# Performance work log

Measured on AMD Instinct MI355X. Metric: run time of the kernel, lower is better.

Reference implementation:

```python
import jax, jax.numpy as jnp
import numpy as np

WS = 8        # window_size
NH = 12       # num_heads


def setup_inputs() -> dict:
    key = jax.random.key(0)
    ks = jax.random.split(key, 9)
    B, C, H, W = 4, 384, 128, 128
    s = 1.0 / np.sqrt(C)
    x = jax.random.normal(ks[0], (B, C, H, W), dtype=jnp.float32)
    Wq = jax.random.normal(ks[1], (C, C), dtype=jnp.float32) * s
    bq = jax.random.normal(ks[2], (C,), dtype=jnp.float32) * 0.01
    Wk = jax.random.normal(ks[3], (C, C), dtype=jnp.float32) * s
    bk = jax.random.normal(ks[4], (C,), dtype=jnp.float32) * 0.01
    Wv = jax.random.normal(ks[5], (C, C), dtype=jnp.float32) * s
    bv = jax.random.normal(ks[6], (C,), dtype=jnp.float32) * 0.01
    Wp = jax.random.normal(ks[7], (C, C), dtype=jnp.float32) * s
    bp = jax.random.normal(ks[8], (C,), dtype=jnp.float32) * 0.01
    return {"x": x, "Wq": Wq, "bq": bq, "Wk": Wk, "bk": bk,
            "Wv": Wv, "bv": bv, "Wp": Wp, "bp": bp}


def reference(x, Wq, bq, Wk, bk, Wv, bv, Wp, bp):
    B, C, H, W = x.shape
    ws2 = WS * WS
    dk = C // NH
    scale = dk ** -0.5

    # window_partition: flat row-major reshape (same semantics as torch's
    # reshape on a contiguous [B,C,H,W] tensor), then permute+view.
    p = x.reshape(B, H // WS, WS, W // WS, WS, C)
    p = jnp.transpose(p, (0, 5, 1, 3, 2, 4))          # [B, C, H/ws, W/ws, ws, ws]
    p = p.reshape(B, C, -1, ws2)                       # [B, C, nW, ws*ws]

    def conv1x1(w, b):  # 1x1 Conv2d on [B,C,nW,ws2]
        return jnp.einsum('bcnw,oc->bonw', p, w) + b[None, :, None, None]

    def heads(t):  # permute(0,2,3,1).contiguous().reshape -> [B, NH, nW, ws2, dk]
        t = jnp.transpose(t, (0, 2, 3, 1))             # [B, nW, ws2, C]
        return t.reshape(B, NH, -1, ws2, dk)           # row-major reinterpretation

    q = heads(conv1x1(Wq, bq))
    k = heads(conv1x1(Wk, bk))
    v = heads(conv1x1(Wv, bv))

    scores = jnp.einsum('bhnqd,bhnkd->bhnqk', q, k) * scale
    attn = jax.nn.softmax(scores, axis=-1)
    o = jnp.einsum('bhnqk,bhnkd->bhnqd', attn, v)      # [B, NH, nW, ws2, dk]
    o = o.reshape(B, -1, ws2, C)                       # [B, nW, ws2, C]

    # window_unpartition
    u = o.reshape(B, -1, WS, WS, C)
    u = jnp.transpose(u, (0, 4, 1, 2, 3))              # [B, C, nW, ws, ws]
    u = u.reshape(B, C, H, W)

    y = jnp.einsum('bchw,oc->bohw', u, Wp) + bp[None, :, None, None]
    return y
```

## Files before the change

### kernel.cpp

```cpp
#include <hip/hip_runtime.h>
#include <hip/hip_bf16.h>
#include <stdint.h>


typedef __bf16 bf16_t;
typedef __bf16 bf16x8 __attribute__((ext_vector_type(8)));
typedef __bf16 bf16x4 __attribute__((ext_vector_type(4)));
typedef float f32x4 __attribute__((ext_vector_type(4)));

__device__ __forceinline__ void gload_lds16(const void* g, void* l) {
  __builtin_amdgcn_global_load_lds((__attribute__((address_space(1))) void*)(g),
                                   (__attribute__((address_space(3))) void*)(l),
                                   16, 0, 0);
}

__global__ __launch_bounds__(256) void prepw_kernel(
    const float* __restrict__ x, bf16_t* __restrict__ Xp,
    const float* __restrict__ wq, const float* __restrict__ wk,
    const float* __restrict__ wv, const float* __restrict__ wp,
    bf16_t* __restrict__ oq, bf16_t* __restrict__ ok,
    bf16_t* __restrict__ ov, bf16_t* __restrict__ op_) {
  if (blockIdx.x < 576) {
    int i = blockIdx.x * 256 + threadIdx.x;
    oq[i] = (bf16_t)wq[i];
    ok[i] = (bf16_t)wk[i];
    ov[i] = (bf16_t)wv[i];
    op_[i] = (bf16_t)wp[i];
    return;
  }
  int gid = (blockIdx.x - 576) * 256 + threadIdx.x;
  int row = gid / 96;
  int c4 = (gid - row * 96) * 4;
  int b = row >> 14;
  int pp = row & 16383;
  int n1 = pp >> 10, n3 = (pp >> 6) & 15, w2 = (pp >> 3) & 7, w4 = pp & 7;
  int P = (n1 << 10) | (w2 << 7) | (n3 << 3) | w4;
  float4 v = *(const float4*)(x + (size_t)((b << 14) | P) * 384 + c4);
  bf16x4 o;
  o[0] = (bf16_t)v.x; o[1] = (bf16_t)v.y; o[2] = (bf16_t)v.z; o[3] = (bf16_t)v.w;
  *(bf16x4*)(Xp + (size_t)row * 384 + c4) = o;
}

__global__ __launch_bounds__(512, 6) void qkv_gemm(
    const bf16_t* __restrict__ Xp, const bf16_t* __restrict__ Wcat,
    const float* __restrict__ bq, const float* __restrict__ bk,
    const float* __restrict__ bv,
    bf16_t* __restrict__ Qs, bf16_t* __restrict__ Ks, bf16_t* __restrict__ Vs) {
  extern __shared__ __align__(16) char smem[];
  const int tid = threadIdx.x;
  const int F = blockIdx.x;
  const int xcd = F & 7;
  const int t = F >> 3;
  const int j = t % 9;
  const int gq = t / 9;
  const int m0 = (gq * 8 + xcd) * 128;
  const int which = j / 3;
  const int cb = (j % 3) * 128;
  const float* bias = which == 0 ? bq : (which == 1 ? bk : bv);
  bf16_t* Out = which == 0 ? Qs : (which == 1 ? Ks : Vs);
  const bf16_t* Arows = Xp + (size_t)m0 * 384;
  const bf16_t* Brows = Wcat + (size_t)j * 128 * 384;

  const int lane = tid & 63, wid = tid >> 6;
  const int l15 = lane & 15, hi = lane >> 4;
  const int wr = wid >> 2, wc = wid & 3;
  const int slot = hi ^ ((l15 >> 1) & 3);

  auto stage = [&](int kt) {
    const int k0 = kt * 32;
    char* base = smem + (kt % 3) * 16384;
    {
      int row = tid >> 2;
      int sg = (tid & 3) ^ ((tid >> 3) & 3);
      gload_lds16(Arows + (size_t)row * 384 + k0 + sg * 8,
                  base + (wid * 64) * 16);
    }
    {
      int row = tid >> 2;
      int sg = (tid & 3) ^ ((tid >> 3) & 3);
      gload_lds16(Brows + (size_t)row * 384 + k0 + sg * 8,
                  base + 8192 + (wid * 64) * 16);
    }
  };

  stage(0); stage(1);
  asm volatile("s_waitcnt vmcnt(2)" ::: "memory");
  __builtin_amdgcn_s_barrier();
  __builtin_amdgcn_sched_barrier(0);

  f32x4 acc[4][2] = {};
#pragma unroll
  for (int kt = 0; kt < 12; ++kt) {
    if (kt > 0) {
      __builtin_amdgcn_s_barrier();
      __builtin_amdgcn_sched_barrier(0);
    }
    if (kt + 2 < 12) stage(kt + 2);
    const char* Ab = smem + (kt % 3) * 16384;
    const char* Bb = Ab + 8192;
    bf16x8 a[4], bfr[2];
#pragma unroll
    for (int i = 0; i < 4; ++i)
      a[i] = *(const bf16x8*)(Ab + (wr * 64 + i * 16 + l15) * 64 + slot * 16);
#pragma unroll
    for (int ni = 0; ni < 2; ++ni)
      bfr[ni] = *(const bf16x8*)(Bb + (wc * 32 + ni * 16 + l15) * 64 + slot * 16);
    __builtin_amdgcn_s_setprio(1);
#pragma unroll
    for (int mi = 0; mi < 4; ++mi)
#pragma unroll
      for (int ni = 0; ni < 2; ++ni)
        acc[mi][ni] = __builtin_amdgcn_mfma_f32_16x16x32_bf16(a[mi], bfr[ni],
                                                              acc[mi][ni], 0, 0, 0);
    __builtin_amdgcn_s_setprio(0);
    if (kt <= 9)       asm volatile("s_waitcnt vmcnt(2)" ::: "memory");
    else if (kt == 10) asm volatile("s_waitcnt vmcnt(0)" ::: "memory");
    __builtin_amdgcn_sched_barrier(0);
  }

#pragma unroll
  for (int ni = 0; ni < 2; ++ni) {
    int chan = cb + wc * 32 + ni * 16 + l15;
    float bv_ = bias[chan];
#pragma unroll
    for (int mi = 0; mi < 4; ++mi)
#pragma unroll
      for (int r = 0; r < 4; ++r) {
        int row = m0 + wr * 64 + mi * 16 + hi * 4 + r;
        Out[(size_t)row * 384 + chan] = (bf16_t)(acc[mi][ni][r] + bv_);
      }
  }
}

__global__ __launch_bounds__(64) void attn_kernel(const bf16_t* __restrict__ Q,
                                                  const bf16_t* __restrict__ K,
                                                  const bf16_t* __restrict__ V,
                                                  bf16_t* __restrict__ O) {
  const size_t base = (size_t)blockIdx.x * 2048;
  const bf16_t* q = Q + base;
  const bf16_t* k = K + base;
  const bf16_t* v = V + base;
  bf16_t* o = O + base;
  const int lane = threadIdx.x;
  const int l15 = lane & 15, hi = lane >> 4;

  __shared__ __align__(16) bf16_t Vt[32][72];
  __shared__ __align__(16) bf16_t Ps[64][72];

#pragma unroll
  for (int j = 0; j < 4; ++j) {
    bf16x8 vv = *(const bf16x8*)(v + lane * 32 + j * 8);
#pragma unroll
    for (int e = 0; e < 8; ++e) Vt[j * 8 + e][lane] = vv[e];
  }

  bf16x8 aQ[4], bK[4];
#pragma unroll
  for (int i = 0; i < 4; ++i) {
    aQ[i] = *(const bf16x8*)(q + (i * 16 + l15) * 32 + hi * 8);
    bK[i] = *(const bf16x8*)(k + (i * 16 + l15) * 32 + hi * 8);
  }
  f32x4 sc[4][4] = {};
#pragma unroll
  for (int mi = 0; mi < 4; ++mi)
#pragma unroll
    for (int ni = 0; ni < 4; ++ni)
      sc[mi][ni] = __builtin_amdgcn_mfma_f32_16x16x32_bf16(aQ[mi], bK[ni],
                                                           sc[mi][ni], 0, 0, 0);

  const float SCALE = 0.17677669529663687f;
  float rs[4][4];
#pragma unroll
  for (int mi = 0; mi < 4; ++mi) {
#pragma unroll
    for (int r = 0; r < 4; ++r) {
      float s0 = sc[mi][0][r] * SCALE, s1 = sc[mi][1][r] * SCALE;
      float s2 = sc[mi][2][r] * SCALE, s3 = sc[mi][3][r] * SCALE;
      float mx = fmaxf(fmaxf(s0, s1), fmaxf(s2, s3));
      mx = fmaxf(mx, __shfl_xor(mx, 1));
      mx = fmaxf(mx, __shfl_xor(mx, 2));
      mx = fmaxf(mx, __shfl_xor(mx, 4));
      mx = fmaxf(mx, __shfl_xor(mx, 8));
      float p0 = __expf(s0 - mx), p1 = __expf(s1 - mx);
      float p2 = __expf(s2 - mx), p3 = __expf(s3 - mx);
      int row = mi * 16 + hi * 4 + r;
      Ps[row][0 + l15] = (bf16_t)p0;
      Ps[row][16 + l15] = (bf16_t)p1;
      Ps[row][32 + l15] = (bf16_t)p2;
      Ps[row][48 + l15] = (bf16_t)p3;
      float sum = p0 + p1 + p2 + p3;
      sum += __shfl_xor(sum, 1);
      sum += __shfl_xor(sum, 2);
      sum += __shfl_xor(sum, 4);
      sum += __shfl_xor(sum, 8);
      rs[mi][r] = sum;
    }
  }
  __syncthreads();

  f32x4 oacc[4][2] = {};
#pragma unroll
  for (int mi = 0; mi < 4; ++mi)
#pragma unroll
    for (int ks = 0; ks < 2; ++ks) {
      bf16x8 aP = *(const bf16x8*)(&Ps[mi * 16 + l15][ks * 32 + hi * 8]);
#pragma unroll
      for (int n2 = 0; n2 < 2; ++n2) {
        bf16x8 bV = *(const bf16x8*)(&Vt[n2 * 16 + l15][ks * 32 + hi * 8]);
        oacc[mi][n2] = __builtin_amdgcn_mfma_f32_16x16x32_bf16(aP, bV,
                                                               oacc[mi][n2], 0, 0, 0);
      }
    }
#pragma unroll
  for (int mi = 0; mi < 4; ++mi)
#pragma unroll
    for (int n2 = 0; n2 < 2; ++n2)
#pragma unroll
      for (int r = 0; r < 4; ++r) {
        int row = mi * 16 + hi * 4 + r;
        o[row * 32 + n2 * 16 + l15] = (bf16_t)(oacc[mi][n2][r] / rs[mi][r]);
      }
}

__global__ __launch_bounds__(512, 6) void proj_gemm(
    const bf16_t* __restrict__ Wpb, const bf16_t* __restrict__ O,
    const float* __restrict__ bp, float* __restrict__ y) {
  extern __shared__ __align__(16) char smem[];
  const int tid = threadIdx.x;
  const int F = blockIdx.x;
  const int xcd = F & 7;
  const int t = F >> 3;
  const int j = t % 3;
  const int gq = t / 3;
  const int g = gq * 8 + xcd;
  const int n0 = (g & 127) * 128;
  const int b = g >> 7;
  const int m0 = j * 128;
  const bf16_t* Arows = Wpb + (size_t)m0 * 384;
  const bf16_t* Brows = O + ((size_t)b * 16384 + n0) * 384;

  const int lane = tid & 63, wid = tid >> 6;
  const int l15 = lane & 15, hi = lane >> 4;
  const int wr = wid >> 2, wc = wid & 3;
  const int slot = hi ^ ((l15 >> 1) & 3);

  auto stage = [&](int kt) {
    const int k0 = kt * 32;
    char* base = smem + (kt % 3) * 16384;
    int row = tid >> 2;
    int sg = (tid & 3) ^ ((tid >> 3) & 3);
    gload_lds16(Arows + (size_t)row * 384 + k0 + sg * 8,
                base + (wid * 64) * 16);
    gload_lds16(Brows + (size_t)row * 384 + k0 + sg * 8,
                base + 8192 + (wid * 64) * 16);
  };

  stage(0); stage(1);
  asm volatile("s_waitcnt vmcnt(2)" ::: "memory");
  __builtin_amdgcn_s_barrier();
  __builtin_amdgcn_sched_barrier(0);

  f32x4 acc[4][2] = {};
#pragma unroll
  for (int kt = 0; kt < 12; ++kt) {
    if (kt > 0) {
      __builtin_amdgcn_s_barrier();
      __builtin_amdgcn_sched_barrier(0);
    }
    if (kt + 2 < 12) stage(kt + 2);
    const char* Ab = smem + (kt % 3) * 16384;
    const char* Bb = Ab + 8192;
    bf16x8 a[4], bfr[2];
#pragma unroll
    for (int i = 0; i < 4; ++i)
      a[i] = *(const bf16x8*)(Ab + (wr * 64 + i * 16 + l15) * 64 + slot * 16);
#pragma unroll
    for (int ni = 0; ni < 2; ++ni)
      bfr[ni] = *(const bf16x8*)(Bb + (wc * 32 + ni * 16 + l15) * 64 + slot * 16);
    __builtin_amdgcn_s_setprio(1);
#pragma unroll
    for (int mi = 0; mi < 4; ++mi)
#pragma unroll
      for (int ni = 0; ni < 2; ++ni)
        acc[mi][ni] = __builtin_amdgcn_mfma_f32_16x16x32_bf16(a[mi], bfr[ni],
                                                              acc[mi][ni], 0, 0, 0);
    __builtin_amdgcn_s_setprio(0);
    if (kt <= 9)       asm volatile("s_waitcnt vmcnt(2)" ::: "memory");
    else if (kt == 10) asm volatile("s_waitcnt vmcnt(0)" ::: "memory");
    __builtin_amdgcn_sched_barrier(0);
  }

  float* yb = y + (size_t)b * 6291456;
#pragma unroll
  for (int mi = 0; mi < 4; ++mi)
#pragma unroll
    for (int r = 0; r < 4; ++r) {
      int och = m0 + wr * 64 + mi * 16 + hi * 4 + r;
      float bpv = bp[och];
#pragma unroll
      for (int ni = 0; ni < 2; ++ni) {
        int pix = n0 + wc * 32 + ni * 16 + l15;
        yb[(size_t)och * 16384 + pix] = acc[mi][ni][r] + bpv;
      }
    }
}

extern "C" void kernel_launch(void* const* d_in, const int* in_sizes, int n_in,
                              void* d_out, int out_size, void* d_ws, size_t ws_size,
                              hipStream_t stream) {
  const float* x  = (const float*)d_in[0];
  const float* Wq = (const float*)d_in[1];
  const float* bq = (const float*)d_in[2];
  const float* Wk = (const float*)d_in[3];
  const float* bk = (const float*)d_in[4];
  const float* Wv = (const float*)d_in[5];
  const float* bv = (const float*)d_in[6];
  const float* Wp = (const float*)d_in[7];
  const float* bp = (const float*)d_in[8];
  float* y = (float*)d_out;

  char* ws = (char*)d_ws;
  const size_t SZ = 50331648;
  bf16_t* Xp  = (bf16_t*)(ws);
  bf16_t* Vs  = (bf16_t*)(ws + SZ);
  bf16_t* Wcat = (bf16_t*)(ws + 2 * SZ);
  bf16_t* Wkb = Wcat + 147456;
  bf16_t* Wvb = Wkb + 147456;
  bf16_t* Wpb = Wvb + 147456;
  bf16_t* Qs  = (bf16_t*)d_out;
  bf16_t* Ks  = (bf16_t*)((char*)d_out + SZ);
  bf16_t* Ob  = Xp;

  prepw_kernel<<<25152, 256, 0, stream>>>(x, Xp, Wq, Wk, Wv, Wp,
                                          Wcat, Wkb, Wvb, Wpb);
  qkv_gemm<<<4608, 512, 49152, stream>>>(Xp, Wcat, bq, bk, bv, Qs, Ks, Vs);
  attn_kernel<<<12288, 64, 0, stream>>>(Qs, Ks, Vs, Ob);
  proj_gemm<<<1536, 512, 49152, stream>>>(Wpb, Ob, bp, y);
}
```

Baseline: 183.3 us.

## Load QKV GEMM A fragments directly from global and halve block size

The QKV GEMM now runs 256-thread blocks of four waves, each wave computing a 64x64 output tile instead of 64x32. Only the weight (B) tile is staged through LDS with the async pipeline, which halves shared memory per block. The activation (A) fragments are read straight from global memory into registers each k-step. This cuts LDS traffic and footprint, but A loads are no longer shared between waves through LDS, so each wave pair re-reads the same rows from global memory. Global-load latency is also exposed inside the loop, and the larger accumulator tile raises register pressure.

```diff
diff --git a/kernel.cpp b/kernel.cpp
--- a/kernel.cpp
+++ b/kernel.cpp
@@ -41,7 +41,7 @@
   *(bf16x4*)(Xp + (size_t)row * 384 + c4) = o;
 }
 
-__global__ __launch_bounds__(512, 6) void qkv_gemm(
+__global__ __launch_bounds__(256, 4) void qkv_gemm(
     const bf16_t* __restrict__ Xp, const bf16_t* __restrict__ Wcat,
     const float* __restrict__ bq, const float* __restrict__ bk,
     const float* __restrict__ bv,
@@ -63,53 +63,50 @@
 
   const int lane = tid & 63, wid = tid >> 6;
   const int l15 = lane & 15, hi = lane >> 4;
-  const int wr = wid >> 2, wc = wid & 3;
-  const int slot = hi ^ ((l15 >> 1) & 3);
-
-  auto stage = [&](int kt) {
+  const int wr = wid >> 1, wc = wid & 1;
+  const int pos = hi ^ ((l15 >> 1) & 3);
+
+  auto stageB = [&](int kt) {
     const int k0 = kt * 32;
-    char* base = smem + (kt % 3) * 16384;
-    {
-      int row = tid >> 2;
-      int sg = (tid & 3) ^ ((tid >> 3) & 3);
-      gload_lds16(Arows + (size_t)row * 384 + k0 + sg * 8,
-                  base + (wid * 64) * 16);
-    }
-    {
-      int row = tid >> 2;
-      int sg = (tid & 3) ^ ((tid >> 3) & 3);
+    char* base = smem + (kt % 3) * 8192;
+#pragma unroll
+    for (int jj = 0; jj < 2; ++jj) {
+      int idx = jj * 256 + tid;
+      int row = idx >> 2;
+      int sg = (idx & 3) ^ ((idx >> 3) & 3);
       gload_lds16(Brows + (size_t)row * 384 + k0 + sg * 8,
-                  base + 8192 + (wid * 64) * 16);
+                  base + (jj * 256 + wid * 64) * 16);
     }
   };
 
-  stage(0); stage(1);
+  stageB(0); stageB(1);
   asm volatile("s_waitcnt vmcnt(2)" ::: "memory");
   __builtin_amdgcn_s_barrier();
   __builtin_amdgcn_sched_barrier(0);
 
-  f32x4 acc[4][2] = {};
+  f32x4 acc[4][4] = {};
 #pragma unroll
   for (int kt = 0; kt < 12; ++kt) {
     if (kt > 0) {
       __builtin_amdgcn_s_barrier();
       __builtin_amdgcn_sched_barrier(0);
     }
-    if (kt + 2 < 12) stage(kt + 2);
-    const char* Ab = smem + (kt % 3) * 16384;
-    const char* Bb = Ab + 8192;
-    bf16x8 a[4], bfr[2];
+    bf16x8 a[4];
 #pragma unroll
     for (int i = 0; i < 4; ++i)
-      a[i] = *(const bf16x8*)(Ab + (wr * 64 + i * 16 + l15) * 64 + slot * 16);
-#pragma unroll
-    for (int ni = 0; ni < 2; ++ni)
-      bfr[ni] = *(const bf16x8*)(Bb + (wc * 32 + ni * 16 + l15) * 64 + slot * 16);
+      a[i] = *(const bf16x8*)(Arows + (size_t)(wr * 64 + i * 16 + l15) * 384 +
+                              kt * 32 + hi * 8);
+    if (kt + 2 < 12) stageB(kt + 2);
+    const char* Bb = smem + (kt % 3) * 8192;
+    bf16x8 bfr[4];
+#pragma unroll
+    for (int ni = 0; ni < 4; ++ni)
+      bfr[ni] = *(const bf16x8*)(Bb + (wc * 64 + ni * 16 + l15) * 64 + pos * 16);
     __builtin_amdgcn_s_setprio(1);
 #pragma unroll
     for (int mi = 0; mi < 4; ++mi)
 #pragma unroll
-      for (int ni = 0; ni < 2; ++ni)
+      for (int ni = 0; ni < 4; ++ni)
         acc[mi][ni] = __builtin_amdgcn_mfma_f32_16x16x32_bf16(a[mi], bfr[ni],
                                                               acc[mi][ni], 0, 0, 0);
     __builtin_amdgcn_s_setprio(0);
@@ -119,8 +116,8 @@
   }
 
 #pragma unroll
-  for (int ni = 0; ni < 2; ++ni) {
-    int chan = cb + wc * 32 + ni * 16 + l15;
+  for (int ni = 0; ni < 4; ++ni) {
+    int chan = cb + wc * 64 + ni * 16 + l15;
     float bv_ = bias[chan];
 #pragma unroll
     for (int mi = 0; mi < 4; ++mi)
@@ -333,7 +330,7 @@
 
   prepw_kernel<<<25152, 256, 0, stream>>>(x, Xp, Wq, Wk, Wv, Wp,
                                           Wcat, Wkb, Wvb, Wpb);
-  qkv_gemm<<<4608, 512, 49152, stream>>>(Xp, Wcat, bq, bk, bv, Qs, Ks, Vs);
+  qkv_gemm<<<4608, 256, 24576, stream>>>(Xp, Wcat, bq, bk, bv, Qs, Ks, Vs);
   attn_kernel<<<12288, 64, 0, stream>>>(Qs, Ks, Vs, Ob);
   proj_gemm<<<1536, 512, 49152, stream>>>(Wpb, Ob, bp, y);
 }
```

Result: slower. 226.1 us (+23.3%).
